# Kernel tuning notes

Hardware: AMD Instinct MI355X
Metric: run time of the kernel (lower is better)

Reference implementation:

```python
import jax, jax.numpy as jnp
import numpy as np

N_HEADS = 16
DIM = 1024
HEAD_DIM = DIM // N_HEADS

def setup_inputs() -> dict:
    key = jax.random.key(0)
    ks = jax.random.split(key, 5)
    B, S = 4, 2048
    x = jax.random.normal(ks[0], (B, S, DIM), dtype=jnp.float32)
    # PyTorch Linear-style params (stored as [in, out] for x @ W)
    sc = 1.0 / np.sqrt(DIM)
    W_qkv = jax.random.uniform(ks[1], (DIM, 3 * DIM), jnp.float32, -sc, sc)
    b_qkv = jax.random.uniform(ks[2], (3 * DIM,), jnp.float32, -sc, sc)
    W_o = jax.random.uniform(ks[3], (DIM, DIM), jnp.float32, -sc, sc)
    b_o = jax.random.uniform(ks[4], (DIM,), jnp.float32, -sc, sc)
    return {"x": x, "W_qkv": W_qkv, "b_qkv": b_qkv, "W_o": W_o, "b_o": b_o}

def reference(x, W_qkv, b_qkv, W_o, b_o):
    B, S, D = x.shape
    qkv = x @ W_qkv + b_qkv                       # [B,S,3D]
    q, k, v = jnp.split(qkv, 3, axis=2)
    # [B,S,D] -> [B,H,S,hd]
    q = q.reshape(B, S, N_HEADS, HEAD_DIM).transpose(0, 2, 1, 3)
    k = k.reshape(B, S, N_HEADS, HEAD_DIM).transpose(0, 2, 1, 3)
    v = v.reshape(B, S, N_HEADS, HEAD_DIM).transpose(0, 2, 1, 3)
    aff = jnp.einsum('bhqd,bhkd->bhqk', q, k) / jnp.sqrt(jnp.float32(HEAD_DIM))
    causal = jnp.tril(jnp.ones((S, S), dtype=bool))  # [S,S]
    aff = jnp.where(causal[None, None], aff, jnp.float32(-jnp.inf))
    attn = jax.nn.softmax(aff, axis=3)
    # dropout p=0.0 (eval): identity
    out = jnp.einsum('bhqk,bhkd->bhqd', attn, v)
    out = out.transpose(0, 2, 1, 3).reshape(B, S, D)
    return out @ W_o + b_o
```

## Files before the change

### kernel.cpp

```cpp
#include <hip/hip_runtime.h>

typedef unsigned short u16;
typedef short bf16x8 __attribute__((ext_vector_type(8)));
typedef float f32x4 __attribute__((ext_vector_type(4)));
typedef unsigned short ushort8v __attribute__((ext_vector_type(8)));
typedef unsigned short us4 __attribute__((ext_vector_type(4)));
typedef float f4v __attribute__((ext_vector_type(4)));

#define LOG2E 1.4426950408889634f
#define FIXMAX_C (12.0f * LOG2E)

static __device__ __forceinline__ float bf2f(u16 h) {
    unsigned int u = ((unsigned int)h) << 16;
    return __builtin_bit_cast(float, u);
}
static __device__ __forceinline__ u16 f2bf(float f) {
    unsigned int u = __builtin_bit_cast(unsigned int, f);
    u += 0x7FFFu + ((u >> 16) & 1u);
    return (u16)(u >> 16);
}
static __device__ __forceinline__ void ld_lds16(const u16* g, u16* l) {
    __builtin_amdgcn_global_load_lds((const __attribute__((address_space(1))) void*)g,
                                     (__attribute__((address_space(3))) void*)l, 16, 0, 0);
}
#define MFMA16(a, b, c) __builtin_amdgcn_mfma_f32_16x16x32_bf16(a, b, c, 0, 0, 0)
#define SW(r, g) (((r) << 6) + ((((g) ^ ((r) & 7))) << 3))

__global__ void cvt_cast(const float* __restrict__ src, u16* __restrict__ dst, int n4) {
    int i = blockIdx.x * blockDim.x + threadIdx.x;
    const int stride = gridDim.x * blockDim.x;
    for (; i < n4; i += stride) {
        f4v v = *(const f4v*)(src + (size_t)i * 4);
        us4 o;
        o[0] = f2bf(v[0]); o[1] = f2bf(v[1]); o[2] = f2bf(v[2]); o[3] = f2bf(v[3]);
        *(us4*)(dst + (size_t)i * 4) = o;
    }
}

__global__ __launch_bounds__(256) void cvt_T(const float* __restrict__ W, u16* __restrict__ WT,
                                             int N, int K) {
    __shared__ u16 tT[64][72];
    const int tid = threadIdx.x;
    const int tiles_n = N >> 6;
    const int tn = blockIdx.x % tiles_n, tk = blockIdx.x / tiles_n;
    const int rr = tid >> 4, c4 = (tid & 15) * 4;
    #pragma unroll
    for (int i = 0; i < 4; i++) {
        int kk = rr + i * 16;
        f4v v = *(const f4v*)&W[(size_t)(tk * 64 + kk) * N + tn * 64 + c4];
        #pragma unroll
        for (int j = 0; j < 4; j++) tT[c4 + j][kk] = f2bf(v[j]);
    }
    __syncthreads();
    const int nrow = tid >> 2, kc = (tid & 3) * 16;
    ushort8v a = *(const ushort8v*)&tT[nrow][kc];
    ushort8v b = *(const ushort8v*)&tT[nrow][kc + 8];
    u16* dst = WT + (size_t)(tn * 64 + nrow) * K + tk * 64 + kc;
    *(ushort8v*)dst = a;
    *(ushort8v*)(dst + 8) = b;
}

#define STG_P0(nb, ts) do {                                      \
    const u16* ga_ = gA + (ts) * 64;                             \
    const u16* gb_ = gB + (ts) * 64;                             \
    u16* la_ = lA + (nb) * 24576;                                \
    u16* lb_ = lB + (nb) * 24576;                                \
    ld_lds16(ga_,      la_);                       \
    ld_lds16(ga_ + 32, la_ + 8192);                \
    ld_lds16(gb_,      lb_);                       \
} while (0)
#define STG_P1(nb, ts) do {                                      \
    const u16* ga_ = gA + 131072 + (ts) * 64;                    \
    const u16* gb_ = gB + (ts) * 64;                             \
    u16* la_ = lA + (nb) * 24576 + 4096;                         \
    u16* lb_ = lB + (nb) * 24576 + 4096;                         \
    ld_lds16(gb_ + 32, lb_);                       \
    ld_lds16(ga_,      la_);                       \
    ld_lds16(ga_ + 32, la_ + 8192);                \
} while (0)

#define PHASE(bufc, qd, DOSTG, STG, VMST) do {                                           \
    bf16x8 paf[4][2]; bf16x8 pbf[2][2];                                                  \
    _Pragma("unroll")                                                                    \
    for (int m_ = 0; m_ < 4; m_++) {                                                     \
        paf[m_][0] = *(const bf16x8*)&sm[(bufc)*24576 + (qd)*4096 + aro + m_*512];       \
        paf[m_][1] = *(const bf16x8*)&sm[(bufc)*24576 + 8192 + (qd)*4096 + aro + m_*512];\
    }                                                                                    \
    _Pragma("unroll")                                                                    \
    for (int n_ = 0; n_ < 2; n_++) {                                                     \
        pbf[n_][0] = *(const bf16x8*)&sm[(bufc)*24576 + 16384 + bro + n_*512];           \
        pbf[n_][1] = *(const bf16x8*)&sm[(bufc)*24576 + 20480 + bro + n_*512];           \
    }                                                                                    \
    if (DOSTG) { STG; }                                                                  \
    asm volatile("" ::: "memory");                                                       \
    __builtin_amdgcn_s_barrier();                                                        \
    asm volatile("s_waitcnt lgkmcnt(0)" ::: "memory");                                   \
    __builtin_amdgcn_sched_barrier(0);                                                   \
    __builtin_amdgcn_s_setprio(1);                                                       \
    _Pragma("unroll")                                                                    \
    for (int m_ = 0; m_ < 4; m_++)                                                       \
        _Pragma("unroll")                                                                \
        for (int n_ = 0; n_ < 2; n_++) {                                                 \
            acc[(qd)*4+m_][n_] = MFMA16(paf[m_][0], pbf[n_][0], acc[(qd)*4+m_][n_]);     \
            acc[(qd)*4+m_][n_] = MFMA16(paf[m_][1], pbf[n_][1], acc[(qd)*4+m_][n_]);     \
        }                                                                                \
    __builtin_amdgcn_s_setprio(0);                                                       \
    VMST;                                                                                \
    __builtin_amdgcn_s_barrier();                                                       \
    asm volatile("" ::: "memory");                                                       \
} while (0)

template <int MODE, int NBX>
__global__ __launch_bounds__(512) void gemm256(
        const u16* __restrict__ A, const u16* __restrict__ BT,
        const float* __restrict__ bias, void* __restrict__ Cout,
        u16* __restrict__ vT) {
    extern __shared__ u16 sm[];
    const int tid = threadIdx.x, lane = tid & 63, wid = tid >> 6;
    const int lm = lane & 15, q = lane >> 4;
    const int wm_id = wid >> 2, wn_id = wid & 3;

    const int id = blockIdx.x;
    const int swz = (id & 7) * (NBX * 4) + (id >> 3);
    const int by = swz / NBX, bx = swz % NBX;
    const int m0 = by * 256, n0 = bx * 128;

    const int sw = (q ^ ((lm >> 1) & 3)) * 8;
    const int aro = (wm_id * 64 + lm) * 32 + sw;
    const int bro = (wn_id * 32 + lm) * 32 + sw;

    const int sw_src = ((lane & 3) ^ ((lane >> 3) & 3)) * 8;
    const int srow = wid * 16 + (lane >> 2);
    const u16* gA = A + (size_t)(m0 + srow) * 1024 + sw_src;
    const u16* gB = BT + (size_t)(n0 + srow) * 1024 + sw_src;
    u16* lA = sm + wid * 512;
    u16* lB = sm + 16384 + wid * 512;

    f32x4 acc[8][2] = {};

    ld_lds16(gA, lA);
    ld_lds16(gA + 32, lA + 8192);
    ld_lds16(gB, lB);
    ld_lds16(gB + 32, lB + 4096);
    ld_lds16(gA + 131072, lA + 4096);
    ld_lds16(gA + 131072 + 32, lA + 8192 + 4096);
    asm volatile("s_waitcnt vmcnt(2)" ::: "memory");
    __builtin_amdgcn_s_barrier();

    #pragma unroll 1
    for (int i = 0; i < 8; ++i) {
        {
            const int t = 2 * i, ts1 = t + 1;
            const bool dostg = (ts1 < 16);
            PHASE(0, 0, dostg, STG_P0(1, ts1),
                  if (t < 15) asm volatile("s_waitcnt vmcnt(3)" ::: "memory");
                  else        asm volatile("s_waitcnt vmcnt(0)" ::: "memory"));
            PHASE(0, 1, dostg, STG_P1(1, ts1),
                  if (t < 15) asm volatile("s_waitcnt vmcnt(2)" ::: "memory"));
        }
        {
            const int t = 2 * i + 1, ts1 = t + 1;
            const bool dostg = (ts1 < 16);
            PHASE(1, 0, dostg, STG_P0(0, ts1),
                  if (t < 15) asm volatile("s_waitcnt vmcnt(3)" ::: "memory");
                  else        asm volatile("s_waitcnt vmcnt(0)" ::: "memory"));
            PHASE(1, 1, dostg, STG_P1(0, ts1),
                  if (t < 15) asm volatile("s_waitcnt vmcnt(2)" ::: "memory"));
        }
    }

    if constexpr (MODE == 0) {
        u16* qkout = (u16*)Cout;
        if (n0 < 2048) {
            #pragma unroll
            for (int ni = 0; ni < 2; ni++) {
                int col = n0 + wn_id * 32 + ni * 16 + lm;
                float bsv = bias[col];
                float sc = (col < 1024) ? 0.125f : 1.0f;
                #pragma unroll
                for (int mi = 0; mi < 8; mi++) {
                    int rowb = m0 + (mi >> 2) * 128 + wm_id * 64 + (mi & 3) * 16 + q * 4;
                    #pragma unroll
                    for (int r = 0; r < 4; r++)
                        qkout[(size_t)(rowb + r) * 2048 + col] = f2bf((acc[mi][ni][r] + bsv) * sc);
                }
            }
        } else {
            const int b_ = m0 >> 11;
            const int sbb = (m0 & 2047);
            #pragma unroll
            for (int ni = 0; ni < 2; ni++) {
                int col = n0 + wn_id * 32 + ni * 16 + lm;
                int hh = (col - 2048) >> 6, dd = (col - 2048) & 63;
                float bsv = bias[col];
                u16* dst = vT + ((size_t)((b_ * 16 + hh) * 64 + dd)) * 2048;
                #pragma unroll
                for (int mi = 0; mi < 8; mi++) {
                    int rw = sbb + (mi >> 2) * 128 + wm_id * 64 + (mi & 3) * 16 + q * 4;
                    us4 pk;
                    #pragma unroll
                    for (int r = 0; r < 4; r++) pk[r] = f2bf(acc[mi][ni][r] + bsv);
                    *(us4*)&dst[rw] = pk;
                }
            }
        }
    } else {
        float* out = (float*)Cout;
        #pragma unroll
        for (int ni = 0; ni < 2; ni++) {
            int col = n0 + wn_id * 32 + ni * 16 + lm;
            float bsv = bias[col];
            #pragma unroll
            for (int mi = 0; mi < 8; mi++) {
                int rowb = m0 + (mi >> 2) * 128 + wm_id * 64 + (mi & 3) * 16 + q * 4;
                #pragma unroll
                for (int r = 0; r < 4; r++)
                    out[(size_t)(rowb + r) * 1024 + col] = acc[mi][ni][r] + bsv;
            }
        }
    }
}

template <bool DIAG>
__device__ __forceinline__ void proc_tile(
        const bf16x8* qf, const u16* __restrict__ ksv, const u16* __restrict__ vsv,
        u16* __restrict__ psw, f32x4* o, f32x4& lacc, const bf16x8 ones,
        int lm, int q, int m0w) {
    f32x4 s[4] = {};
    __builtin_amdgcn_s_setprio(1);
    #pragma unroll
    for (int g2 = 0; g2 < 2; g2++) {
        bf16x8 a = qf[g2];
        #pragma unroll
        for (int nt = 0; nt < 4; nt++) {
            bf16x8 bb = *(const bf16x8*)&ksv[SW(nt * 16 + lm, q + 4 * g2)];
            s[nt] = MFMA16(a, bb, s[nt]);
        }
    }
    __builtin_amdgcn_s_setprio(0);
    #pragma unroll
    for (int nt = 0; nt < 4; nt++)
        #pragma unroll
        for (int r = 0; r < 4; r++) {
            float v = s[nt][r];
            if constexpr (DIAG) {
                if (nt * 16 + lm > m0w + q * 4 + r) v = -3e30f;
            }
            float pv = __builtin_amdgcn_exp2f(v * LOG2E - FIXMAX_C);
            unsigned int uu = __builtin_bit_cast(unsigned int, pv);
            psw[SW(q * 4 + r, 2 * nt + (lm >> 3)) + (lm & 7)] = (u16)(uu >> 16);
        }
    __builtin_amdgcn_s_setprio(1);
    #pragma unroll
    for (int g2 = 0; g2 < 2; g2++) {
        bf16x8 ap = *(const bf16x8*)&psw[SW(lm, q + 4 * g2)];
        lacc = MFMA16(ap, ones, lacc);
        #pragma unroll
        for (int nt = 0; nt < 4; nt++) {
            bf16x8 bv = *(const bf16x8*)&vsv[SW(nt * 16 + lm, q + 4 * g2)];
            o[nt] = MFMA16(ap, bv, o[nt]);
        }
    }
    __builtin_amdgcn_s_setprio(0);
}

__global__ __launch_bounds__(256, 2) void attn3(
        const u16* __restrict__ qk, const u16* __restrict__ vT, u16* __restrict__ aw) {
    __shared__ u16 smem[16384];
    u16* ks = smem;
    u16* vs = smem + 4096;
    const int tid = threadIdx.x, lane = tid & 63, wid = tid >> 6;
    const int lm = lane & 15, q = lane >> 4;
    const int bh = blockIdx.x, p = blockIdx.y;
    const int b = bh >> 4, h = bh & 15;
    const int t[4] = {p, 15 - p, 16 + p, 31 - p};
    const size_t rowbase = (size_t)b * 2048;
    const int lr = tid >> 2, lcg = (tid & 3) * 2, lc = (tid & 3) * 16;
    const int m0w = wid * 16;
    u16* psw0 = smem + 8192 + wid * 1024;
    u16* psw1 = smem + 12288 + wid * 1024;

    bf16x8 ones;
    #pragma unroll
    for (int j = 0; j < 8; j++) ones[j] = (short)0x3F80;

    #pragma unroll
    for (int i = 0; i < 4; i++) {
        const u16* qa = qk + (rowbase + t[i] * 64 + lr) * 2048 + h * 64 + lc;
        *(ushort8v*)&smem[i * 4096 + SW(lr, lcg)]     = *(const ushort8v*)qa;
        *(ushort8v*)&smem[i * 4096 + SW(lr, lcg + 1)] = *(const ushort8v*)(qa + 8);
    }
    __syncthreads();
    bf16x8 qf[4][2];
    #pragma unroll
    for (int i = 0; i < 4; i++)
        #pragma unroll
        for (int g2 = 0; g2 < 2; g2++)
            qf[i][g2] = *(const bf16x8*)&smem[i * 4096 + SW(m0w + lm, q + 4 * g2)];

    f32x4 o[4][4] = {};
    f32x4 lacc[4] = {};

    const u16* kg = qk + (rowbase + lr) * 2048 + 1024 + h * 64 + lc;
    const u16* vg = vT + ((size_t)bh * 64 + lr) * 2048 + lc;
    const int jmax = t[3];

    ushort8v k0 = *(const ushort8v*)kg, k1 = *(const ushort8v*)(kg + 8);
    ushort8v v0 = *(const ushort8v*)vg, v1 = *(const ushort8v*)(vg + 8);

    for (int jt = 0; jt <= jmax; ++jt) {
        __syncthreads();
        *(ushort8v*)&ks[SW(lr, lcg)] = k0; *(ushort8v*)&ks[SW(lr, lcg + 1)] = k1;
        *(ushort8v*)&vs[SW(lr, lcg)] = v0; *(ushort8v*)&vs[SW(lr, lcg + 1)] = v1;
        __syncthreads();
        if (jt < jmax) {
            const u16* kgj = kg + (size_t)(jt + 1) * 64 * 2048;
            const u16* vgj = vg + (jt + 1) * 64;
            k0 = *(const ushort8v*)kgj; k1 = *(const ushort8v*)(kgj + 8);
            v0 = *(const ushort8v*)vgj; v1 = *(const ushort8v*)(vgj + 8);
        }
        #pragma unroll
        for (int i = 0; i < 4; i++) {
            u16* pswi = (i & 1) ? psw1 : psw0;
            if (jt < t[i])
                proc_tile<false>(qf[i], ks, vs, pswi, o[i], lacc[i], ones, lm, q, m0w);
            else if (jt == t[i])
                proc_tile<true>(qf[i], ks, vs, pswi, o[i], lacc[i], ones, lm, q, m0w);
        }
    }

    #pragma unroll
    for (int i = 0; i < 4; i++) {
        f32x4 li;
        #pragma unroll
        for (int r = 0; r < 4; r++) li[r] = __builtin_amdgcn_rcpf(lacc[i][r]);
        #pragma unroll
        for (int nt = 0; nt < 4; nt++)
            #pragma unroll
            for (int r = 0; r < 4; r++) {
                int row = t[i] * 64 + m0w + q * 4 + r;
                int col = h * 64 + nt * 16 + lm;
                aw[(rowbase + row) * 1024 + col] = f2bf(o[i][nt][r] * li[r]);
            }
    }
}

extern "C" void kernel_launch(void* const* d_in, const int* in_sizes, int n_in,
                              void* d_out, int out_size, void* d_ws, size_t ws_size,
                              hipStream_t stream) {
    const float* x    = (const float*)d_in[0];
    const float* Wqkv = (const float*)d_in[1];
    const float* bqkv = (const float*)d_in[2];
    const float* Wo   = (const float*)d_in[3];
    const float* bo   = (const float*)d_in[4];
    float* out = (float*)d_out;

    u16* xb     = (u16*)d_ws;
    u16* WqkvT  = xb + (size_t)8192 * 1024;
    u16* WoT    = WqkvT + (size_t)3072 * 1024;
    u16* qk     = WoT + (size_t)1024 * 1024;
    u16* vT     = qk + (size_t)8192 * 2048;
    u16* aw     = vT + (size_t)64 * 64 * 2048;

    static bool attr_done = false;
    if (!attr_done) {
        hipFuncSetAttribute(reinterpret_cast<const void*>(gemm256<0, 24>),
                            hipFuncAttributeMaxDynamicSharedMemorySize, 98304);
        hipFuncSetAttribute(reinterpret_cast<const void*>(gemm256<1, 8>),
                            hipFuncAttributeMaxDynamicSharedMemorySize, 98304);
        attr_done = true;
    }

    cvt_cast<<<2048, 256, 0, stream>>>(x, xb, 8192 * 1024 / 4);
    cvt_T<<<48 * 16, 256, 0, stream>>>(Wqkv, WqkvT, 3072, 1024);
    cvt_T<<<16 * 16, 256, 0, stream>>>(Wo, WoT, 1024, 1024);

    gemm256<0, 24><<<768, 512, 98304, stream>>>(xb, WqkvT, bqkv, qk, vT);
    attn3<<<dim3(64, 8), 256, 0, stream>>>(qk, vT, aw);
    gemm256<1, 8><<<256, 512, 98304, stream>>>(aw, WoT, bo, out, nullptr);
}
```

Measured before the change: 252.0 us.

## Use 128x128 tile GEMM for output projection and fold log2e into Q scale

The output projection GEMM moves from the 256x128 tile, 512-thread kernel to a new simpler 128x128 tile, 256-thread kernel with static double-half LDS staging, launching 512 blocks instead of 256 for better CU fill. The QKV epilogue now multiplies Q by 0.125*log2e, so the attention softmax can call exp2 directly without the per-element multiply and the fixed-max offset. Removing the fixed-max subtraction changes the numeric range of the exponentials and risks overflow for large scores. The new GEMM has no software pipelining and synchronizes twice per K step.

```diff
diff --git a/kernel.cpp b/kernel.cpp
--- a/kernel.cpp
+++ b/kernel.cpp
@@ -8,7 +8,6 @@
 typedef float f4v __attribute__((ext_vector_type(4)));
 
 #define LOG2E 1.4426950408889634f
-#define FIXMAX_C (12.0f * LOG2E)
 
 static __device__ __forceinline__ float bf2f(u16 h) {
     unsigned int u = ((unsigned int)h) << 16;
@@ -110,15 +109,15 @@
     asm volatile("" ::: "memory");                                                       \
 } while (0)
 
-template <int MODE, int NBX>
-__global__ __launch_bounds__(512) void gemm256(
+__global__ __launch_bounds__(512) void gemm256qkv(
         const u16* __restrict__ A, const u16* __restrict__ BT,
-        const float* __restrict__ bias, void* __restrict__ Cout,
+        const float* __restrict__ bias, u16* __restrict__ qkout,
         u16* __restrict__ vT) {
     extern __shared__ u16 sm[];
     const int tid = threadIdx.x, lane = tid & 63, wid = tid >> 6;
     const int lm = lane & 15, q = lane >> 4;
     const int wm_id = wid >> 2, wn_id = wid & 3;
+    const int NBX = 24;
 
     const int id = blockIdx.x;
     const int swz = (id & 7) * (NBX * 4) + (id >> 3);
@@ -169,55 +168,96 @@
         }
     }
 
-    if constexpr (MODE == 0) {
-        u16* qkout = (u16*)Cout;
-        if (n0 < 2048) {
-            #pragma unroll
-            for (int ni = 0; ni < 2; ni++) {
-                int col = n0 + wn_id * 32 + ni * 16 + lm;
-                float bsv = bias[col];
-                float sc = (col < 1024) ? 0.125f : 1.0f;
-                #pragma unroll
-                for (int mi = 0; mi < 8; mi++) {
-                    int rowb = m0 + (mi >> 2) * 128 + wm_id * 64 + (mi & 3) * 16 + q * 4;
-                    #pragma unroll
-                    for (int r = 0; r < 4; r++)
-                        qkout[(size_t)(rowb + r) * 2048 + col] = f2bf((acc[mi][ni][r] + bsv) * sc);
-                }
-            }
-        } else {
-            const int b_ = m0 >> 11;
-            const int sbb = (m0 & 2047);
-            #pragma unroll
-            for (int ni = 0; ni < 2; ni++) {
-                int col = n0 + wn_id * 32 + ni * 16 + lm;
-                int hh = (col - 2048) >> 6, dd = (col - 2048) & 63;
-                float bsv = bias[col];
-                u16* dst = vT + ((size_t)((b_ * 16 + hh) * 64 + dd)) * 2048;
-                #pragma unroll
-                for (int mi = 0; mi < 8; mi++) {
-                    int rw = sbb + (mi >> 2) * 128 + wm_id * 64 + (mi & 3) * 16 + q * 4;
-                    us4 pk;
-                    #pragma unroll
-                    for (int r = 0; r < 4; r++) pk[r] = f2bf(acc[mi][ni][r] + bsv);
-                    *(us4*)&dst[rw] = pk;
-                }
-            }
-        }
-    } else {
-        float* out = (float*)Cout;
+    if (n0 < 2048) {
         #pragma unroll
         for (int ni = 0; ni < 2; ni++) {
             int col = n0 + wn_id * 32 + ni * 16 + lm;
             float bsv = bias[col];
+            float sc = (col < 1024) ? (0.125f * LOG2E) : 1.0f;
             #pragma unroll
             for (int mi = 0; mi < 8; mi++) {
                 int rowb = m0 + (mi >> 2) * 128 + wm_id * 64 + (mi & 3) * 16 + q * 4;
                 #pragma unroll
                 for (int r = 0; r < 4; r++)
-                    out[(size_t)(rowb + r) * 1024 + col] = acc[mi][ni][r] + bsv;
-            }
-        }
+                    qkout[(size_t)(rowb + r) * 2048 + col] = f2bf((acc[mi][ni][r] + bsv) * sc);
+            }
+        }
+    } else {
+        const int b_ = m0 >> 11;
+        const int sbb = (m0 & 2047);
+        #pragma unroll
+        for (int ni = 0; ni < 2; ni++) {
+            int col = n0 + wn_id * 32 + ni * 16 + lm;
+            int hh = (col - 2048) >> 6, dd = (col - 2048) & 63;
+            float bsv = bias[col];
+            u16* dst = vT + ((size_t)((b_ * 16 + hh) * 64 + dd)) * 2048;
+            #pragma unroll
+            for (int mi = 0; mi < 8; mi++) {
+                int rw = sbb + (mi >> 2) * 128 + wm_id * 64 + (mi & 3) * 16 + q * 4;
+                us4 pk;
+                #pragma unroll
+                for (int r = 0; r < 4; r++) pk[r] = f2bf(acc[mi][ni][r] + bsv);
+                *(us4*)&dst[rw] = pk;
+            }
+        }
+    }
+}
+
+__global__ __launch_bounds__(256) void gemm128o(
+        const u16* __restrict__ A, const u16* __restrict__ BT,
+        const float* __restrict__ bias, float* __restrict__ out,
+        int K, int nx) {
+    __shared__ u16 As[2][128][32];
+    __shared__ u16 Bs[2][128][32];
+    const int tid = threadIdx.x, lane = tid & 63, wid = tid >> 6;
+    const int lm = lane & 15, q = lane >> 4;
+    const int id = blockIdx.x;
+    const int panel = id / (nx * 8), rem = id % (nx * 8);
+    const int bx = rem >> 3, by = panel * 8 + (rem & 7);
+    const int m0 = by * 128, n0 = bx * 128;
+    const int wm = (wid >> 1) * 64, wn = (wid & 1) * 64;
+    const int w32 = wid * 32;
+    f32x4 acc[4][4] = {};
+
+    const u16* gA = A + (size_t)(m0 + w32 + (lane >> 2)) * K + (lane & 3) * 8;
+    const u16* gB = BT + (size_t)(n0 + w32 + (lane >> 2)) * K + (lane & 3) * 8;
+
+    for (int kb = 0; kb < K; kb += 64) {
+        __syncthreads();
+        #pragma unroll
+        for (int h = 0; h < 2; h++)
+            #pragma unroll
+            for (int i = 0; i < 2; i++) {
+                ld_lds16(gA + kb + h * 32 + (size_t)i * 16 * K, &As[h][w32 + i * 16][0]);
+                ld_lds16(gB + kb + h * 32 + (size_t)i * 16 * K, &Bs[h][w32 + i * 16][0]);
+            }
+        __syncthreads();
+        #pragma unroll
+        for (int kk = 0; kk < 2; kk++) {
+            bf16x8 af[4], bfr[4];
+            #pragma unroll
+            for (int mi = 0; mi < 4; mi++) af[mi] = *(const bf16x8*)&As[kk][wm + mi * 16 + lm][q * 8];
+            #pragma unroll
+            for (int ni = 0; ni < 4; ni++) bfr[ni] = *(const bf16x8*)&Bs[kk][wn + ni * 16 + lm][q * 8];
+            #pragma unroll
+            for (int mi = 0; mi < 4; mi++)
+                #pragma unroll
+                for (int ni = 0; ni < 4; ni++)
+                    acc[mi][ni] = MFMA16(af[mi], bfr[ni], acc[mi][ni]);
+        }
+    }
+
+    #pragma unroll
+    for (int ni = 0; ni < 4; ni++) {
+        int col = n0 + wn + ni * 16 + lm;
+        float bsv = bias[col];
+        #pragma unroll
+        for (int mi = 0; mi < 4; mi++)
+            #pragma unroll
+            for (int r = 0; r < 4; r++) {
+                int row = m0 + wm + mi * 16 + q * 4 + r;
+                out[(size_t)row * 1024 + col] = acc[mi][ni][r] + bsv;
+            }
     }
 }
 
@@ -246,7 +286,7 @@
             if constexpr (DIAG) {
                 if (nt * 16 + lm > m0w + q * 4 + r) v = -3e30f;
             }
-            float pv = __builtin_amdgcn_exp2f(v * LOG2E - FIXMAX_C);
+            float pv = __builtin_amdgcn_exp2f(v);
             unsigned int uu = __builtin_bit_cast(unsigned int, pv);
             psw[SW(q * 4 + r, 2 * nt + (lm >> 3)) + (lm & 7)] = (u16)(uu >> 16);
         }
@@ -364,9 +404,7 @@
 
     static bool attr_done = false;
     if (!attr_done) {
-        hipFuncSetAttribute(reinterpret_cast<const void*>(gemm256<0, 24>),
-                            hipFuncAttributeMaxDynamicSharedMemorySize, 98304);
-        hipFuncSetAttribute(reinterpret_cast<const void*>(gemm256<1, 8>),
+        hipFuncSetAttribute(reinterpret_cast<const void*>(gemm256qkv),
                             hipFuncAttributeMaxDynamicSharedMemorySize, 98304);
         attr_done = true;
     }
@@ -375,7 +413,7 @@
     cvt_T<<<48 * 16, 256, 0, stream>>>(Wqkv, WqkvT, 3072, 1024);
     cvt_T<<<16 * 16, 256, 0, stream>>>(Wo, WoT, 1024, 1024);
 
-    gemm256<0, 24><<<768, 512, 98304, stream>>>(xb, WqkvT, bqkv, qk, vT);
+    gemm256qkv<<<768, 512, 98304, stream>>>(xb, WqkvT, bqkv, qk, vT);
     attn3<<<dim3(64, 8), 256, 0, stream>>>(qk, vT, aw);
-    gemm256<1, 8><<<256, 512, 98304, stream>>>(aw, WoT, bo, out, nullptr);
-}
+    gemm128o<<<8 * 64, 256, 0, stream>>>(aw, WoT, bo, out, 1024, 8);
+}
```

Result: no change. 250.5 us (-0.6%).
